# Kernel optimization log

Measured on AMD Instinct MI355X. Metric: run time of the kernel, lower is better.

The kernel has to match this reference:

```python
import jax, jax.numpy as jnp
import numpy as np

N_NODES = 50000
N_EDGES = 800000
N_GRAPHS = 64
D_IN, D_HID, D_OUT = 128, 128, 64


def setup_inputs() -> dict:
    key = jax.random.key(0)
    ks = jax.random.split(key, 9)
    s = 0.05
    return {
        "x": jax.random.normal(ks[0], (N_NODES, D_IN), jnp.float32),
        "edge_index": jax.random.randint(ks[1], (2, N_EDGES), 0, N_NODES, dtype=jnp.int64),
        "batch": jnp.sort(jax.random.randint(ks[2], (N_NODES,), 0, N_GRAPHS, dtype=jnp.int64)),
        "W1": jax.random.normal(ks[3], (D_IN, D_HID), jnp.float32) * s,
        "b1": jnp.zeros((D_HID,), jnp.float32),
        "W2": jax.random.normal(ks[4], (D_HID, D_HID), jnp.float32) * s,
        "b2": jnp.zeros((D_HID,), jnp.float32),
        "W3": jax.random.normal(ks[5], (D_HID, D_OUT), jnp.float32) * s,
        "b3": jnp.zeros((D_OUT,), jnp.float32),
    }


def _gcn_conv(x, W, b, src, dst, dinv, n_nodes):
    # PyG GCNConv: h = X W; out = sum_{j->i} norm_ij h_j + self-loop term + b
    h = x @ W
    norm_e = dinv[src] * dinv[dst]                      # [E]
    agg = jax.ops.segment_sum(norm_e[:, None] * h[src], dst, num_segments=n_nodes)
    agg = agg + (dinv * dinv)[:, None] * h              # self-loop (norm = dinv_i^2)
    return agg + b


def reference(x, edge_index, batch, W1, b1, W2, b2, W3, b3):
    n_nodes = x.shape[0]
    src, dst = edge_index[0], edge_index[1]
    # symmetric normalization with self-loops: deg_i = in_degree_i + 1
    deg = jax.ops.segment_sum(jnp.ones_like(dst, dtype=x.dtype), dst, num_segments=n_nodes) + 1.0
    dinv = jax.lax.rsqrt(deg)

    h = jax.nn.relu(_gcn_conv(x, W1, b1, src, dst, dinv, n_nodes))
    h = jax.nn.relu(_gcn_conv(h, W2, b2, src, dst, dinv, n_nodes))
    h = _gcn_conv(h, W3, b3, src, dst, dinv, n_nodes)

    # global_mean_pool over graph id
    sums = jax.ops.segment_sum(h, batch, num_segments=N_GRAPHS)
    counts = jax.ops.segment_sum(jnp.ones((n_nodes,), h.dtype), batch, num_segments=N_GRAPHS)
    return sums / jnp.maximum(counts, 1.0)[:, None]
```

## Files before the change

kernel.cpp:

```cpp
#include <hip/hip_runtime.h>

#define NN 50000
#define NE 800000
#define NG 64
#define NCHUNK 64
#define CHUNK 12500
#define HALF 25000

typedef short short8 __attribute__((ext_vector_type(8)));
typedef float f32x4 __attribute__((ext_vector_type(4)));

__device__ __forceinline__ unsigned short f2bf(float f) {
    unsigned int u = __float_as_uint(f);
    u = (u + 0x7FFFu + ((u >> 16) & 1u)) >> 16;
    return (unsigned short)u;
}
__device__ __forceinline__ float bf2f(unsigned short h) {
    return __uint_as_float((unsigned int)h << 16);
}

__global__ __launch_bounds__(1024) void k_hist(const int* __restrict__ ei,
                                               unsigned short* __restrict__ rank,
                                               unsigned short* __restrict__ percnt) {
    __shared__ unsigned int cnt[HALF / 2];
    const int b = blockIdx.x;
    const int dbase = blockIdx.y * HALF;
    const int tid = threadIdx.x;
    for (int i = tid; i < HALF / 2; i += 1024) cnt[i] = 0;
    __syncthreads();
    const int e0 = b * CHUNK;
    for (int i = tid; i < CHUNK; i += 1024) {
        const int d = ei[NE + e0 + i];
        const int local = d - dbase;
        if ((unsigned)local < (unsigned)HALF) {
            const unsigned int old = atomicAdd(&cnt[local >> 1], 1u << ((local & 1) * 16));
            rank[e0 + i] = (unsigned short)((old >> ((local & 1) * 16)) & 0xFFFFu);
        }
    }
    __syncthreads();
    unsigned int* dst = (unsigned int*)&percnt[(size_t)b * NN + dbase];
    for (int i = tid; i < HALF / 2; i += 1024) dst[i] = cnt[i];
}

__global__ __launch_bounds__(256) void k_colscan(unsigned short* __restrict__ percnt,
                                                 int* __restrict__ degcnt) {
    const int d = blockIdx.x * 256 + threadIdx.x;
    if (d >= NN) return;
    int acc = 0;
#pragma unroll 8
    for (int b = 0; b < NCHUNK; ++b) {
        const int c = percnt[(size_t)b * NN + d];
        percnt[(size_t)b * NN + d] = (unsigned short)acc;
        acc += c;
    }
    degcnt[d] = acc;
}

__global__ __launch_bounds__(256) void k_dinv(const int* __restrict__ degcnt, float* __restrict__ dinv) {
    int i = blockIdx.x * 256 + threadIdx.x;
    if (i < NN) dinv[i] = (float)(1.0 / sqrt((double)degcnt[i] + 1.0));
}

__global__ __launch_bounds__(1024) void k_scan1(const int* __restrict__ cnt, int* __restrict__ row_ptr,
                                                int* __restrict__ blk_sums) {
    __shared__ int s[1024];
    const int tid = threadIdx.x;
    const int i = blockIdx.x * 1024 + tid;
    int v = (i < NN) ? cnt[i] : 0;
    s[tid] = v;
    __syncthreads();
    for (int off = 1; off < 1024; off <<= 1) {
        int t = (tid >= off) ? s[tid - off] : 0;
        __syncthreads();
        s[tid] += t;
        __syncthreads();
    }
    if (i < NN) row_ptr[i] = s[tid] - v;
    if (tid == 1023) blk_sums[blockIdx.x] = s[1023];
}

__global__ __launch_bounds__(64) void k_scan2(int* __restrict__ blk_sums, int nb) {
    int l = threadIdx.x;
    int v = (l < nb) ? blk_sums[l] : 0;
    int incl = v;
    for (int off = 1; off < 64; off <<= 1) {
        int t = __shfl_up(incl, off, 64);
        if (l >= off) incl += t;
    }
    if (l < nb) blk_sums[l] = incl - v;
}

__global__ __launch_bounds__(1024) void k_scan3(int* __restrict__ row_ptr, const int* __restrict__ blk_sums) {
    int i = blockIdx.x * 1024 + threadIdx.x;
    if (i < NN) row_ptr[i] += blk_sums[blockIdx.x];
    if (i == 0) row_ptr[NN] = NE;
}

__global__ __launch_bounds__(256) void k_fill3(const int* __restrict__ ei, const int* __restrict__ row_ptr,
                                               const unsigned short* __restrict__ rank,
                                               const unsigned short* __restrict__ offs,
                                               int* __restrict__ csr_src) {
    const int e = blockIdx.x * 256 + threadIdx.x;
    if (e >= NE) return;
    const int s = ei[e];
    const int d = ei[NE + e];
    const int b = e / CHUNK;
    const int pos = row_ptr[d] + (int)offs[(size_t)b * NN + d] + (int)rank[e];
    csr_src[pos] = s;
}

template <int DO>
__global__ __launch_bounds__(256) void k_gemm_mfma(const float* __restrict__ A, const float* __restrict__ W,
                                                   unsigned short* __restrict__ C, int M) {
    constexpr int NT = DO / 16;
    constexpr int LDK = 136;
    __shared__ __align__(16) unsigned short As[64 * LDK];
    __shared__ __align__(16) unsigned short Wt[DO * LDK];
    const int tid = threadIdx.x;
    const int row0 = blockIdx.x * 64;

    for (int task = tid; task < 64 * (DO / 4); task += 256) {
        const int k0 = (task / (DO / 4)) * 2;
        const int n4 = (task % (DO / 4)) * 4;
        const float4 wa = *(const float4*)&W[(size_t)k0 * DO + n4];
        const float4 wb = *(const float4*)&W[(size_t)(k0 + 1) * DO + n4];
        const float pa[4] = {wa.x, wa.y, wa.z, wa.w};
        const float pb[4] = {wb.x, wb.y, wb.z, wb.w};
#pragma unroll
        for (int i = 0; i < 4; ++i) {
            const unsigned int pk = (unsigned int)f2bf(pa[i]) | ((unsigned int)f2bf(pb[i]) << 16);
            *(unsigned int*)&Wt[(n4 + i) * LDK + k0] = pk;
        }
    }
    {
        const int r = tid >> 2;
        const int ks = (tid & 3) * 32;
        const int grow = row0 + r;
#pragma unroll
        for (int q = 0; q < 8; ++q) {
            float4 v = make_float4(0.f, 0.f, 0.f, 0.f);
            if (grow < M) v = *(const float4*)&A[(size_t)grow * 128 + ks + q * 4];
            const unsigned long long pk =
                (unsigned long long)f2bf(v.x) | ((unsigned long long)f2bf(v.y) << 16) |
                ((unsigned long long)f2bf(v.z) << 32) | ((unsigned long long)f2bf(v.w) << 48);
            *(unsigned long long*)&As[r * LDK + ks + q * 4] = pk;
        }
    }
    __syncthreads();

    const int l = tid & 63;
    const int w = tid >> 6;
    const int lr = l & 15;
    const int lg = l >> 4;
    f32x4 acc[NT];
#pragma unroll
    for (int nt = 0; nt < NT; ++nt) acc[nt] = (f32x4){0.f, 0.f, 0.f, 0.f};

#pragma unroll
    for (int kk = 0; kk < 128; kk += 32) {
        const short8 af = *(const short8*)&As[(w * 16 + lr) * LDK + kk + lg * 8];
#pragma unroll
        for (int nt = 0; nt < NT; ++nt) {
            const short8 bfv = *(const short8*)&Wt[(nt * 16 + lr) * LDK + kk + lg * 8];
            acc[nt] = __builtin_amdgcn_mfma_f32_16x16x32_bf16(af, bfv, acc[nt], 0, 0, 0);
        }
    }

#pragma unroll
    for (int nt = 0; nt < NT; ++nt) {
#pragma unroll
        for (int r = 0; r < 4; ++r) {
            const int grow = row0 + w * 16 + lg * 4 + r;
            if (grow < M) C[(size_t)grow * DO + nt * 16 + lr] = f2bf(acc[nt][r]);
        }
    }
}

template <int D, bool RELU>
__global__ __launch_bounds__(256) void k_agg(const unsigned short* __restrict__ T, const float* __restrict__ bias,
                                             const float* __restrict__ dinv, const int* __restrict__ row_ptr,
                                             const int* __restrict__ csr_src,
                                             float* __restrict__ out) {
    constexpr int G = D / 4;
    constexpr int NPB = 256 / G;
    const int tid = threadIdx.x;
    const int lane = tid % G;
    const int grp = tid / G;
    const int n = blockIdx.x * NPB + grp;
    if (n >= NN) return;

    const float di_n = dinv[n];
    double a0 = 0.0, a1 = 0.0, a2 = 0.0, a3 = 0.0;
    const int beg = row_ptr[n];
    const int end = row_ptr[n + 1];
    int e = beg;
    for (; e + 4 <= end; e += 4) {
        const int s0 = csr_src[e + 0], s1 = csr_src[e + 1], s2 = csr_src[e + 2], s3 = csr_src[e + 3];
        const float w0 = dinv[s0] * di_n, w1 = dinv[s1] * di_n, w2 = dinv[s2] * di_n, w3 = dinv[s3] * di_n;
        const ushort4 v0 = *(const ushort4*)&T[(size_t)s0 * D + lane * 4];
        const ushort4 v1 = *(const ushort4*)&T[(size_t)s1 * D + lane * 4];
        const ushort4 v2 = *(const ushort4*)&T[(size_t)s2 * D + lane * 4];
        const ushort4 v3 = *(const ushort4*)&T[(size_t)s3 * D + lane * 4];
        a0 += (double)w0 * bf2f(v0.x) + (double)w1 * bf2f(v1.x) + (double)w2 * bf2f(v2.x) + (double)w3 * bf2f(v3.x);
        a1 += (double)w0 * bf2f(v0.y) + (double)w1 * bf2f(v1.y) + (double)w2 * bf2f(v2.y) + (double)w3 * bf2f(v3.y);
        a2 += (double)w0 * bf2f(v0.z) + (double)w1 * bf2f(v1.z) + (double)w2 * bf2f(v2.z) + (double)w3 * bf2f(v3.z);
        a3 += (double)w0 * bf2f(v0.w) + (double)w1 * bf2f(v1.w) + (double)w2 * bf2f(v2.w) + (double)w3 * bf2f(v3.w);
    }
    for (; e < end; ++e) {
        const int s = csr_src[e];
        const float w = dinv[s] * di_n;
        const ushort4 v = *(const ushort4*)&T[(size_t)s * D + lane * 4];
        a0 += (double)w * bf2f(v.x);
        a1 += (double)w * bf2f(v.y);
        a2 += (double)w * bf2f(v.z);
        a3 += (double)w * bf2f(v.w);
    }
    {
        const double w = (double)di_n * (double)di_n;
        const ushort4 v = *(const ushort4*)&T[(size_t)n * D + lane * 4];
        a0 += w * bf2f(v.x);
        a1 += w * bf2f(v.y);
        a2 += w * bf2f(v.z);
        a3 += w * bf2f(v.w);
    }
    const float4 b = *(const float4*)&bias[lane * 4];
    a0 += b.x; a1 += b.y; a2 += b.z; a3 += b.w;
    float4 r;
    r.x = (float)a0; r.y = (float)a1; r.z = (float)a2; r.w = (float)a3;
    if (RELU) {
        r.x = fmaxf(r.x, 0.f);
        r.y = fmaxf(r.y, 0.f);
        r.z = fmaxf(r.z, 0.f);
        r.w = fmaxf(r.w, 0.f);
    }
    *(float4*)&out[(size_t)n * D + lane * 4] = r;
}

__global__ __launch_bounds__(256) void k_pool(const float* __restrict__ h, const int* __restrict__ batch,
                                              double* __restrict__ sums, int* __restrict__ cnts) {
    const int NB = 256;
    const int n0 = blockIdx.x * NB;
    const int d = threadIdx.x & 63;
    const int sub = threadIdx.x >> 6;
    double acc = 0.0;
    int cnt = 0;
    int cur = -1;
    for (int i = sub; i < NB; i += 4) {
        int n = n0 + i;
        if (n >= NN) break;
        int g = batch[n];
        if (g != cur) {
            if (cur >= 0) {
                atomicAdd(&sums[cur * 64 + d], acc);
                if (d == 0) atomicAdd(&cnts[cur], cnt);
            }
            cur = g;
            acc = 0.0;
            cnt = 0;
        }
        acc += (double)h[(size_t)n * 64 + d];
        cnt++;
    }
    if (cur >= 0) {
        atomicAdd(&sums[cur * 64 + d], acc);
        if (d == 0) atomicAdd(&cnts[cur], cnt);
    }
}

__global__ __launch_bounds__(256) void k_final(const double* __restrict__ sums, const int* __restrict__ cnts,
                                               float* __restrict__ out) {
    int i = blockIdx.x * 256 + threadIdx.x;
    if (i >= NG * 64) return;
    int g = i >> 6;
    double c = (double)max(cnts[g], 1);
    out[i] = (float)(sums[i] / c);
}

extern "C" void kernel_launch(void* const* d_in, const int* in_sizes, int n_in,
                              void* d_out, int out_size, void* d_ws, size_t ws_size,
                              hipStream_t stream) {
    (void)in_sizes; (void)n_in; (void)out_size; (void)ws_size;
    const float* x     = (const float*)d_in[0];
    const int*   ei    = (const int*)d_in[1];
    const int*   batch = (const int*)d_in[2];
    const float* W1    = (const float*)d_in[3];
    const float* b1    = (const float*)d_in[4];
    const float* W2    = (const float*)d_in[5];
    const float* b2    = (const float*)d_in[6];
    const float* W3    = (const float*)d_in[7];
    const float* b3    = (const float*)d_in[8];
    float* out = (float*)d_out;

    char* w = (char*)d_ws;
    char*  zbase = w;
    double* psums  = (double*)w;        w += (size_t)NG * 64 * 8;
    int*    pcnts  = (int*)w;           w += 256;
    size_t zbytes = (size_t)(w - zbase);
    int*    degcnt = (int*)w;           w += (size_t)NN * 4;
    float*  dinv   = (float*)w;         w += (size_t)NN * 4;
    int*    row_ptr = (int*)w;          w += (size_t)(NN + 4) * 4;
    int*    blk_sums = (int*)w;         w += 64 * 4;
    unsigned short* rank   = (unsigned short*)w;  w += (size_t)NE * 2;
    unsigned short* percnt = (unsigned short*)w;  w += (size_t)NCHUNK * NN * 2;
    int*    csr_src = (int*)w;          w += (size_t)NE * 4;
    unsigned short* bufT = (unsigned short*)w;  w += (size_t)NN * 128 * 2;
    float* bufA = (float*)w;            w += (size_t)NN * 128 * 4;

    hipMemsetAsync(zbase, 0, zbytes, stream);

    k_hist<<<dim3(NCHUNK, 2), 1024, 0, stream>>>(ei, rank, percnt);
    k_colscan<<<(NN + 255) / 256, 256, 0, stream>>>(percnt, degcnt);
    k_dinv<<<(NN + 255) / 256, 256, 0, stream>>>(degcnt, dinv);
    const int nb_scan = (NN + 1023) / 1024;
    k_scan1<<<nb_scan, 1024, 0, stream>>>(degcnt, row_ptr, blk_sums);
    k_scan2<<<1, 64, 0, stream>>>(blk_sums, nb_scan);
    k_scan3<<<nb_scan, 1024, 0, stream>>>(row_ptr, blk_sums);
    k_fill3<<<(NE + 255) / 256, 256, 0, stream>>>(ei, row_ptr, rank, percnt, csr_src);

    const int gemm_grid = (NN + 63) / 64;
    k_gemm_mfma<128><<<gemm_grid, 256, 0, stream>>>(x, W1, bufT, NN);
    k_agg<128, true><<<(NN + 7) / 8, 256, 0, stream>>>(bufT, b1, dinv, row_ptr, csr_src, bufA);
    k_gemm_mfma<128><<<gemm_grid, 256, 0, stream>>>(bufA, W2, bufT, NN);
    k_agg<128, true><<<(NN + 7) / 8, 256, 0, stream>>>(bufT, b2, dinv, row_ptr, csr_src, bufA);
    k_gemm_mfma<64><<<gemm_grid, 256, 0, stream>>>(bufA, W3, bufT, NN);
    k_agg<64, false><<<(NN + 15) / 16, 256, 0, stream>>>(bufT, b3, dinv, row_ptr, csr_src, bufA);
    k_pool<<<(NN + 255) / 256, 256, 0, stream>>>(bufA, batch, psums, pcnts);
    k_final<<<(NG * 64 + 255) / 256, 256, 0, stream>>>(psums, pcnts, out);
}
```

Before: 252.8 us.

## Split aggregation into 32-feature column chunks mapped across XCDs; fuse dinv into colscan

The aggregation kernel now has each block handle one 32-feature slice (64 bytes per row) for 32 nodes. The low 3 bits of the block index pick the feature chunk and node slot, so consecutive blocks, which likely land on different XCDs, each touch a distinct column slice of T. The aim is to shrink each XCD's gather working set so it fits in its L2. Separately, the dinv computation is folded into the column-scan kernel, removing one launch. The trade-off is that row_ptr, csr_src and dinv are now reread once per feature chunk, and each gather is only 64 bytes wide.

```diff
diff --git a/kernel.cpp b/kernel.cpp
--- a/kernel.cpp
+++ b/kernel.cpp
@@ -43,7 +43,7 @@
 }
 
 __global__ __launch_bounds__(256) void k_colscan(unsigned short* __restrict__ percnt,
-                                                 int* __restrict__ degcnt) {
+                                                 int* __restrict__ degcnt, float* __restrict__ dinv) {
     const int d = blockIdx.x * 256 + threadIdx.x;
     if (d >= NN) return;
     int acc = 0;
@@ -54,11 +54,7 @@
         acc += c;
     }
     degcnt[d] = acc;
-}
-
-__global__ __launch_bounds__(256) void k_dinv(const int* __restrict__ degcnt, float* __restrict__ dinv) {
-    int i = blockIdx.x * 256 + threadIdx.x;
-    if (i < NN) dinv[i] = (float)(1.0 / sqrt((double)degcnt[i] + 1.0));
+    dinv[d] = (float)(1.0 / sqrt((double)acc + 1.0));
 }
 
 __global__ __launch_bounds__(1024) void k_scan1(const int* __restrict__ cnt, int* __restrict__ row_ptr,
@@ -181,13 +177,19 @@
                                              const float* __restrict__ dinv, const int* __restrict__ row_ptr,
                                              const int* __restrict__ csr_src,
                                              float* __restrict__ out) {
-    constexpr int G = D / 4;
-    constexpr int NPB = 256 / G;
+    constexpr int CH = D / 32;
+    constexpr int XPC = 8 / CH;
+    constexpr int NPS = NN / XPC;
+    const int sub = blockIdx.x & 7;
+    const int chunk = sub / XPC;
+    const int slot = sub % XPC;
+    const int nb = blockIdx.x >> 3;
     const int tid = threadIdx.x;
-    const int lane = tid % G;
-    const int grp = tid / G;
-    const int n = blockIdx.x * NPB + grp;
-    if (n >= NN) return;
+    const int lane = tid & 7;
+    const int grp = tid >> 3;
+    const int n = slot * NPS + nb * 32 + grp;
+    if (n >= slot * NPS + NPS || n >= NN) return;
+    const int f0 = chunk * 32 + lane * 4;
 
     const float di_n = dinv[n];
     double a0 = 0.0, a1 = 0.0, a2 = 0.0, a3 = 0.0;
@@ -197,10 +199,10 @@
     for (; e + 4 <= end; e += 4) {
         const int s0 = csr_src[e + 0], s1 = csr_src[e + 1], s2 = csr_src[e + 2], s3 = csr_src[e + 3];
         const float w0 = dinv[s0] * di_n, w1 = dinv[s1] * di_n, w2 = dinv[s2] * di_n, w3 = dinv[s3] * di_n;
-        const ushort4 v0 = *(const ushort4*)&T[(size_t)s0 * D + lane * 4];
-        const ushort4 v1 = *(const ushort4*)&T[(size_t)s1 * D + lane * 4];
-        const ushort4 v2 = *(const ushort4*)&T[(size_t)s2 * D + lane * 4];
-        const ushort4 v3 = *(const ushort4*)&T[(size_t)s3 * D + lane * 4];
+        const ushort4 v0 = *(const ushort4*)&T[(size_t)s0 * D + f0];
+        const ushort4 v1 = *(const ushort4*)&T[(size_t)s1 * D + f0];
+        const ushort4 v2 = *(const ushort4*)&T[(size_t)s2 * D + f0];
+        const ushort4 v3 = *(const ushort4*)&T[(size_t)s3 * D + f0];
         a0 += (double)w0 * bf2f(v0.x) + (double)w1 * bf2f(v1.x) + (double)w2 * bf2f(v2.x) + (double)w3 * bf2f(v3.x);
         a1 += (double)w0 * bf2f(v0.y) + (double)w1 * bf2f(v1.y) + (double)w2 * bf2f(v2.y) + (double)w3 * bf2f(v3.y);
         a2 += (double)w0 * bf2f(v0.z) + (double)w1 * bf2f(v1.z) + (double)w2 * bf2f(v2.z) + (double)w3 * bf2f(v3.z);
@@ -209,7 +211,7 @@
     for (; e < end; ++e) {
         const int s = csr_src[e];
         const float w = dinv[s] * di_n;
-        const ushort4 v = *(const ushort4*)&T[(size_t)s * D + lane * 4];
+        const ushort4 v = *(const ushort4*)&T[(size_t)s * D + f0];
         a0 += (double)w * bf2f(v.x);
         a1 += (double)w * bf2f(v.y);
         a2 += (double)w * bf2f(v.z);
@@ -217,13 +219,13 @@
     }
     {
         const double w = (double)di_n * (double)di_n;
-        const ushort4 v = *(const ushort4*)&T[(size_t)n * D + lane * 4];
+        const ushort4 v = *(const ushort4*)&T[(size_t)n * D + f0];
         a0 += w * bf2f(v.x);
         a1 += w * bf2f(v.y);
         a2 += w * bf2f(v.z);
         a3 += w * bf2f(v.w);
     }
-    const float4 b = *(const float4*)&bias[lane * 4];
+    const float4 b = *(const float4*)&bias[f0];
     a0 += b.x; a1 += b.y; a2 += b.z; a3 += b.w;
     float4 r;
     r.x = (float)a0; r.y = (float)a1; r.z = (float)a2; r.w = (float)a3;
@@ -233,7 +235,7 @@
         r.z = fmaxf(r.z, 0.f);
         r.w = fmaxf(r.w, 0.f);
     }
-    *(float4*)&out[(size_t)n * D + lane * 4] = r;
+    *(float4*)&out[(size_t)n * D + f0] = r;
 }
 
 __global__ __launch_bounds__(256) void k_pool(const float* __restrict__ h, const int* __restrict__ batch,
@@ -309,8 +311,7 @@
     hipMemsetAsync(zbase, 0, zbytes, stream);
 
     k_hist<<<dim3(NCHUNK, 2), 1024, 0, stream>>>(ei, rank, percnt);
-    k_colscan<<<(NN + 255) / 256, 256, 0, stream>>>(percnt, degcnt);
-    k_dinv<<<(NN + 255) / 256, 256, 0, stream>>>(degcnt, dinv);
+    k_colscan<<<(NN + 255) / 256, 256, 0, stream>>>(percnt, degcnt, dinv);
     const int nb_scan = (NN + 1023) / 1024;
     k_scan1<<<nb_scan, 1024, 0, stream>>>(degcnt, row_ptr, blk_sums);
     k_scan2<<<1, 64, 0, stream>>>(blk_sums, nb_scan);
@@ -318,12 +319,14 @@
     k_fill3<<<(NE + 255) / 256, 256, 0, stream>>>(ei, row_ptr, rank, percnt, csr_src);
 
     const int gemm_grid = (NN + 63) / 64;
+    const int agg_grid128 = 8 * ((25000 + 31) / 32);
+    const int agg_grid64  = 8 * ((12500 + 31) / 32);
     k_gemm_mfma<128><<<gemm_grid, 256, 0, stream>>>(x, W1, bufT, NN);
-    k_agg<128, true><<<(NN + 7) / 8, 256, 0, stream>>>(bufT, b1, dinv, row_ptr, csr_src, bufA);
+    k_agg<128, true><<<agg_grid128, 256, 0, stream>>>(bufT, b1, dinv, row_ptr, csr_src, bufA);
     k_gemm_mfma<128><<<gemm_grid, 256, 0, stream>>>(bufA, W2, bufT, NN);
-    k_agg<128, true><<<(NN + 7) / 8, 256, 0, stream>>>(bufT, b2, dinv, row_ptr, csr_src, bufA);
+    k_agg<128, true><<<agg_grid128, 256, 0, stream>>>(bufT, b2, dinv, row_ptr, csr_src, bufA);
     k_gemm_mfma<64><<<gemm_grid, 256, 0, stream>>>(bufA, W3, bufT, NN);
-    k_agg<64, false><<<(NN + 15) / 16, 256, 0, stream>>>(bufT, b3, dinv, row_ptr, csr_src, bufA);
+    k_agg<64, false><<<agg_grid64, 256, 0, stream>>>(bufT, b3, dinv, row_ptr, csr_src, bufA);
     k_pool<<<(NN + 255) / 256, 256, 0, stream>>>(bufA, batch, psums, pcnts);
     k_final<<<(NG * 64 + 255) / 256, 256, 0, stream>>>(psums, pcnts, out);
 }
```

After: 348.8 us. 38.0% more time.

## Store aggregation outputs as bf16, use fp32 accumulation and wider gathers

Applied to the files above, without the earlier changes.

Aggregation kernels now write bf16 activations instead of fp32, and the next GEMM loads them directly without conversion. The last layer's pooling reads the bf16 output. Accumulation switches from double to fp32 FMAs, with 8 features per thread via 16-byte gathers. The dinv kernel is folded into the column scan. This cuts intermediate memory traffic, the cost of double-precision arithmetic and one launch, in exchange for lower precision in the stored activations and the accumulation.

```diff
diff --git a/kernel.cpp b/kernel.cpp
--- a/kernel.cpp
+++ b/kernel.cpp
@@ -17,6 +17,17 @@
 }
 __device__ __forceinline__ float bf2f(unsigned short h) {
     return __uint_as_float((unsigned int)h << 16);
+}
+__device__ __forceinline__ void fma8(float* acc, float w, const uint4 v) {
+    const unsigned int u0 = v.x, u1 = v.y, u2 = v.z, u3 = v.w;
+    acc[0] = fmaf(w, __uint_as_float(u0 << 16), acc[0]);
+    acc[1] = fmaf(w, __uint_as_float(u0 & 0xFFFF0000u), acc[1]);
+    acc[2] = fmaf(w, __uint_as_float(u1 << 16), acc[2]);
+    acc[3] = fmaf(w, __uint_as_float(u1 & 0xFFFF0000u), acc[3]);
+    acc[4] = fmaf(w, __uint_as_float(u2 << 16), acc[4]);
+    acc[5] = fmaf(w, __uint_as_float(u2 & 0xFFFF0000u), acc[5]);
+    acc[6] = fmaf(w, __uint_as_float(u3 << 16), acc[6]);
+    acc[7] = fmaf(w, __uint_as_float(u3 & 0xFFFF0000u), acc[7]);
 }
 
 __global__ __launch_bounds__(1024) void k_hist(const int* __restrict__ ei,
@@ -43,7 +54,7 @@
 }
 
 __global__ __launch_bounds__(256) void k_colscan(unsigned short* __restrict__ percnt,
-                                                 int* __restrict__ degcnt) {
+                                                 int* __restrict__ degcnt, float* __restrict__ dinv) {
     const int d = blockIdx.x * 256 + threadIdx.x;
     if (d >= NN) return;
     int acc = 0;
@@ -54,11 +65,7 @@
         acc += c;
     }
     degcnt[d] = acc;
-}
-
-__global__ __launch_bounds__(256) void k_dinv(const int* __restrict__ degcnt, float* __restrict__ dinv) {
-    int i = blockIdx.x * 256 + threadIdx.x;
-    if (i < NN) dinv[i] = (float)(1.0 / sqrt((double)degcnt[i] + 1.0));
+    dinv[d] = (float)(1.0 / sqrt((double)acc + 1.0));
 }
 
 __global__ __launch_bounds__(1024) void k_scan1(const int* __restrict__ cnt, int* __restrict__ row_ptr,
@@ -109,8 +116,8 @@
     csr_src[pos] = s;
 }
 
-template <int DO>
-__global__ __launch_bounds__(256) void k_gemm_mfma(const float* __restrict__ A, const float* __restrict__ W,
+template <int DO, bool AF32>
+__global__ __launch_bounds__(256) void k_gemm_mfma(const void* __restrict__ Ain, const float* __restrict__ W,
                                                    unsigned short* __restrict__ C, int M) {
     constexpr int NT = DO / 16;
     constexpr int LDK = 136;
@@ -132,7 +139,8 @@
             *(unsigned int*)&Wt[(n4 + i) * LDK + k0] = pk;
         }
     }
-    {
+    if constexpr (AF32) {
+        const float* A = (const float*)Ain;
         const int r = tid >> 2;
         const int ks = (tid & 3) * 32;
         const int grow = row0 + r;
@@ -145,6 +153,17 @@
                 ((unsigned long long)f2bf(v.z) << 32) | ((unsigned long long)f2bf(v.w) << 48);
             *(unsigned long long*)&As[r * LDK + ks + q * 4] = pk;
         }
+    } else {
+        const unsigned short* A = (const unsigned short*)Ain;
+        const int r = tid >> 2;
+        const int c0 = (tid & 3) * 32;
+        const int grow = row0 + r;
+#pragma unroll
+        for (int q = 0; q < 4; ++q) {
+            uint4 v = make_uint4(0, 0, 0, 0);
+            if (grow < M) v = *(const uint4*)&A[(size_t)grow * 128 + c0 + q * 8];
+            *(uint4*)&As[r * LDK + c0 + q * 8] = v;
+        }
     }
     __syncthreads();
 
@@ -180,63 +199,60 @@
 __global__ __launch_bounds__(256) void k_agg(const unsigned short* __restrict__ T, const float* __restrict__ bias,
                                              const float* __restrict__ dinv, const int* __restrict__ row_ptr,
                                              const int* __restrict__ csr_src,
-                                             float* __restrict__ out) {
-    constexpr int G = D / 4;
+                                             unsigned short* __restrict__ out) {
+    constexpr int G = D / 8;
     constexpr int NPB = 256 / G;
     const int tid = threadIdx.x;
     const int lane = tid % G;
     const int grp = tid / G;
     const int n = blockIdx.x * NPB + grp;
     if (n >= NN) return;
+    const int f0 = lane * 8;
 
     const float di_n = dinv[n];
-    double a0 = 0.0, a1 = 0.0, a2 = 0.0, a3 = 0.0;
+    float acc[8] = {0.f, 0.f, 0.f, 0.f, 0.f, 0.f, 0.f, 0.f};
     const int beg = row_ptr[n];
     const int end = row_ptr[n + 1];
     int e = beg;
     for (; e + 4 <= end; e += 4) {
         const int s0 = csr_src[e + 0], s1 = csr_src[e + 1], s2 = csr_src[e + 2], s3 = csr_src[e + 3];
         const float w0 = dinv[s0] * di_n, w1 = dinv[s1] * di_n, w2 = dinv[s2] * di_n, w3 = dinv[s3] * di_n;
-        const ushort4 v0 = *(const ushort4*)&T[(size_t)s0 * D + lane * 4];
-        const ushort4 v1 = *(const ushort4*)&T[(size_t)s1 * D + lane * 4];
-        const ushort4 v2 = *(const ushort4*)&T[(size_t)s2 * D + lane * 4];
-        const ushort4 v3 = *(const ushort4*)&T[(size_t)s3 * D + lane * 4];
-        a0 += (double)w0 * bf2f(v0.x) + (double)w1 * bf2f(v1.x) + (double)w2 * bf2f(v2.x) + (double)w3 * bf2f(v3.x);
-        a1 += (double)w0 * bf2f(v0.y) + (double)w1 * bf2f(v1.y) + (double)w2 * bf2f(v2.y) + (double)w3 * bf2f(v3.y);
-        a2 += (double)w0 * bf2f(v0.z) + (double)w1 * bf2f(v1.z) + (double)w2 * bf2f(v2.z) + (double)w3 * bf2f(v3.z);
-        a3 += (double)w0 * bf2f(v0.w) + (double)w1 * bf2f(v1.w) + (double)w2 * bf2f(v2.w) + (double)w3 * bf2f(v3.w);
+        const uint4 v0 = *(const uint4*)&T[(size_t)s0 * D + f0];
+        const uint4 v1 = *(const uint4*)&T[(size_t)s1 * D + f0];
+        const uint4 v2 = *(const uint4*)&T[(size_t)s2 * D + f0];
+        const uint4 v3 = *(const uint4*)&T[(size_t)s3 * D + f0];
+        fma8(acc, w0, v0);
+        fma8(acc, w1, v1);
+        fma8(acc, w2, v2);
+        fma8(acc, w3, v3);
     }
     for (; e < end; ++e) {
         const int s = csr_src[e];
         const float w = dinv[s] * di_n;
-        const ushort4 v = *(const ushort4*)&T[(size_t)s * D + lane * 4];
-        a0 += (double)w * bf2f(v.x);
-        a1 += (double)w * bf2f(v.y);
-        a2 += (double)w * bf2f(v.z);
-        a3 += (double)w * bf2f(v.w);
+        const uint4 v = *(const uint4*)&T[(size_t)s * D + f0];
+        fma8(acc, w, v);
     }
     {
-        const double w = (double)di_n * (double)di_n;
-        const ushort4 v = *(const ushort4*)&T[(size_t)n * D + lane * 4];
-        a0 += w * bf2f(v.x);
-        a1 += w * bf2f(v.y);
-        a2 += w * bf2f(v.z);
-        a3 += w * bf2f(v.w);
-    }
-    const float4 b = *(const float4*)&bias[lane * 4];
-    a0 += b.x; a1 += b.y; a2 += b.z; a3 += b.w;
-    float4 r;
-    r.x = (float)a0; r.y = (float)a1; r.z = (float)a2; r.w = (float)a3;
+        const uint4 v = *(const uint4*)&T[(size_t)n * D + f0];
+        fma8(acc, di_n * di_n, v);
+    }
+    const float4 b0 = *(const float4*)&bias[f0];
+    const float4 b1 = *(const float4*)&bias[f0 + 4];
+    acc[0] += b0.x; acc[1] += b0.y; acc[2] += b0.z; acc[3] += b0.w;
+    acc[4] += b1.x; acc[5] += b1.y; acc[6] += b1.z; acc[7] += b1.w;
     if (RELU) {
-        r.x = fmaxf(r.x, 0.f);
-        r.y = fmaxf(r.y, 0.f);
-        r.z = fmaxf(r.z, 0.f);
-        r.w = fmaxf(r.w, 0.f);
-    }
-    *(float4*)&out[(size_t)n * D + lane * 4] = r;
-}
-
-__global__ __launch_bounds__(256) void k_pool(const float* __restrict__ h, const int* __restrict__ batch,
+#pragma unroll
+        for (int j = 0; j < 8; ++j) acc[j] = fmaxf(acc[j], 0.f);
+    }
+    uint4 o;
+    o.x = (unsigned int)f2bf(acc[0]) | ((unsigned int)f2bf(acc[1]) << 16);
+    o.y = (unsigned int)f2bf(acc[2]) | ((unsigned int)f2bf(acc[3]) << 16);
+    o.z = (unsigned int)f2bf(acc[4]) | ((unsigned int)f2bf(acc[5]) << 16);
+    o.w = (unsigned int)f2bf(acc[6]) | ((unsigned int)f2bf(acc[7]) << 16);
+    *(uint4*)&out[(size_t)n * D + f0] = o;
+}
+
+__global__ __launch_bounds__(256) void k_pool(const unsigned short* __restrict__ h, const int* __restrict__ batch,
                                               double* __restrict__ sums, int* __restrict__ cnts) {
     const int NB = 256;
     const int n0 = blockIdx.x * NB;
@@ -258,7 +274,7 @@
             acc = 0.0;
             cnt = 0;
         }
-        acc += (double)h[(size_t)n * 64 + d];
+        acc += (double)bf2f(h[(size_t)n * 64 + d]);
         cnt++;
     }
     if (cur >= 0) {
@@ -304,13 +320,12 @@
     unsigned short* percnt = (unsigned short*)w;  w += (size_t)NCHUNK * NN * 2;
     int*    csr_src = (int*)w;          w += (size_t)NE * 4;
     unsigned short* bufT = (unsigned short*)w;  w += (size_t)NN * 128 * 2;
-    float* bufA = (float*)w;            w += (size_t)NN * 128 * 4;
+    unsigned short* bufA = (unsigned short*)w;  w += (size_t)NN * 128 * 2;
 
     hipMemsetAsync(zbase, 0, zbytes, stream);
 
     k_hist<<<dim3(NCHUNK, 2), 1024, 0, stream>>>(ei, rank, percnt);
-    k_colscan<<<(NN + 255) / 256, 256, 0, stream>>>(percnt, degcnt);
-    k_dinv<<<(NN + 255) / 256, 256, 0, stream>>>(degcnt, dinv);
+    k_colscan<<<(NN + 255) / 256, 256, 0, stream>>>(percnt, degcnt, dinv);
     const int nb_scan = (NN + 1023) / 1024;
     k_scan1<<<nb_scan, 1024, 0, stream>>>(degcnt, row_ptr, blk_sums);
     k_scan2<<<1, 64, 0, stream>>>(blk_sums, nb_scan);
@@ -318,12 +333,14 @@
     k_fill3<<<(NE + 255) / 256, 256, 0, stream>>>(ei, row_ptr, rank, percnt, csr_src);
 
     const int gemm_grid = (NN + 63) / 64;
-    k_gemm_mfma<128><<<gemm_grid, 256, 0, stream>>>(x, W1, bufT, NN);
-    k_agg<128, true><<<(NN + 7) / 8, 256, 0, stream>>>(bufT, b1, dinv, row_ptr, csr_src, bufA);
-    k_gemm_mfma<128><<<gemm_grid, 256, 0, stream>>>(bufA, W2, bufT, NN);
-    k_agg<128, true><<<(NN + 7) / 8, 256, 0, stream>>>(bufT, b2, dinv, row_ptr, csr_src, bufA);
-    k_gemm_mfma<64><<<gemm_grid, 256, 0, stream>>>(bufA, W3, bufT, NN);
-    k_agg<64, false><<<(NN + 15) / 16, 256, 0, stream>>>(bufT, b3, dinv, row_ptr, csr_src, bufA);
+    const int agg_grid128 = (NN + 15) / 16;
+    const int agg_grid64  = (NN + 31) / 32;
+    k_gemm_mfma<128, true><<<gemm_grid, 256, 0, stream>>>(x, W1, bufT, NN);
+    k_agg<128, true><<<agg_grid128, 256, 0, stream>>>(bufT, b1, dinv, row_ptr, csr_src, bufA);
+    k_gemm_mfma<128, false><<<gemm_grid, 256, 0, stream>>>(bufA, W2, bufT, NN);
+    k_agg<128, true><<<agg_grid128, 256, 0, stream>>>(bufT, b2, dinv, row_ptr, csr_src, bufA);
+    k_gemm_mfma<64, false><<<gemm_grid, 256, 0, stream>>>(bufA, W3, bufT, NN);
+    k_agg<64, false><<<agg_grid64, 256, 0, stream>>>(bufT, b3, dinv, row_ptr, csr_src, bufA);
     k_pool<<<(NN + 255) / 256, 256, 0, stream>>>(bufA, batch, psums, pcnts);
     k_final<<<(NG * 64 + 255) / 256, 256, 0, stream>>>(psums, pcnts, out);
 }
```

New measurement: 238.2 us. 1.06x faster.
